# Kernel tuning notes

Hardware: AMD Instinct MI355X
Metric: run time of the kernel (lower is better)

Reference implementation:

```python
import jax, jax.numpy as jnp
import numpy as np

COLUMN_COUNT = 2048
CELLS_PER_COLUMN = 32
NUM_CELLS = COLUMN_COUNT * CELLS_PER_COLUMN
MAX_SEGMENTS = 16
MAX_SYNAPSES = 32
ACTIVATION_THRESHOLD = 13
PERMANENCE_CONNECTED = 0.5


def setup_inputs() -> dict:
    key = jax.random.key(0)
    k1, k2, k3, k4, k5 = jax.random.split(key, 5)
    active_columns = jax.random.randint(k1, (COLUMN_COUNT,), 0, 2).astype(jnp.float32)
    prev_active = jax.random.randint(k2, (NUM_CELLS,), 0, 2).astype(jnp.float32)
    prev_predictive = jax.random.randint(k3, (NUM_CELLS,), 0, 2).astype(jnp.float32)
    seg_pre = jax.random.randint(k4, (NUM_CELLS, MAX_SEGMENTS, MAX_SYNAPSES), 0, NUM_CELLS, dtype=jnp.int32)
    seg_perm = jax.random.uniform(k5, (NUM_CELLS, MAX_SEGMENTS, MAX_SYNAPSES), dtype=jnp.float32)
    return {
        'active_columns': active_columns,
        'prev_active': prev_active,
        'prev_predictive': prev_predictive,
        'seg_pre': seg_pre,
        'seg_perm': seg_perm,
    }


def _best_segment_activity(seg_pre, connected, active_vec):
    """Per cell: max over segments of (# synapses that are connected AND whose
    presynaptic cell is active). Mirrors _get_segment_activity/_get_best_matching_segment."""
    pre_active = active_vec[seg_pre] > 0          # [N, S, K] irregular gather
    counts = jnp.sum(connected & pre_active, axis=-1)  # [N, S]
    return jnp.max(counts, axis=-1)               # [N]


def reference(active_columns, prev_active, prev_predictive, seg_pre, seg_perm):
    C, cpc = COLUMN_COUNT, CELLS_PER_COLUMN
    connected = seg_perm >= PERMANENCE_CONNECTED   # [N, S, K]

    col_active = active_columns > 0                           # [C]
    pred = (prev_predictive > 0).reshape(C, cpc)              # [C, cpc]
    col_has_pred = jnp.any(pred, axis=1)                      # [C]

    # Active cells: predicted cells if any prediction in column, else burst (all cells).
    new_active = jnp.where(col_active[:, None],
                           jnp.where(col_has_pred[:, None], pred, True),
                           False)                             # [C, cpc]
    active_flat = new_active.reshape(-1).astype(jnp.float32)  # [N]

    # New predictive cells: any segment with activity >= activation_threshold
    # w.r.t. the NEW active set.
    best_act = _best_segment_activity(seg_pre, connected, active_flat)  # [N]
    new_predictive = (best_act >= ACTIVATION_THRESHOLD).astype(jnp.float32)

    # Anomaly: fraction of active columns with no predicted cell.
    n_active_cols = jnp.sum(col_active)
    n_predicted = jnp.sum(col_active & col_has_pred)
    anomaly = (1.0 - n_predicted / jnp.maximum(n_active_cols, 1)).astype(jnp.float32)

    return active_flat, new_predictive, anomaly


if __name__ == '__main__':
    out = reference(**setup_inputs())
    print([o.shape for o in out])
```

## Files before the change

kernel.cpp:

```cpp
#include <hip/hip_runtime.h>

#define COLS    2048
#define CPC     32
#define NCELLS  65536
#define SEGS    16
#define SYN     32
#define THRESH  13

#define CPW     16
#define CPB     (4 * CPW)
#define PREDICT_GRID (NCELLS / CPB)

__global__ __launch_bounds__(256) void tm_active_kernel(
    const float* __restrict__ active_columns,
    const float* __restrict__ prev_predictive,
    float* __restrict__ out_active,
    unsigned int* __restrict__ ws_mask,
    unsigned char* __restrict__ ws_flags)
{
    int n = blockIdx.x * 256 + threadIdx.x;
    int c = n >> 5;
    int j = n & 31;
    int lane = threadIdx.x & 63;

    bool predbit    = prev_predictive[n] > 0.0f;
    bool col_active = active_columns[c] > 0.0f;

    unsigned long long pb = __ballot(predbit);
    unsigned int colmask = (lane < 32) ? (unsigned int)pb : (unsigned int)(pb >> 32);
    bool has_pred = (colmask != 0u);

    bool active = col_active && (has_pred ? predbit : true);
    out_active[n] = active ? 1.0f : 0.0f;

    unsigned long long ab = __ballot(active);
    if (lane == 0)  ws_mask[c] = (unsigned int)ab;
    if (lane == 32) ws_mask[c] = (unsigned int)(ab >> 32);

    if (j == 0)
        ws_flags[c] = (unsigned char)((col_active ? 1 : 0) |
                                      ((col_active && has_pred) ? 2 : 0));
}

typedef const __attribute__((address_space(1))) void* gas_ptr;
typedef __attribute__((address_space(3)))       void* las_ptr;

__device__ __forceinline__ void dma_1kb(const char* g, char* lds, int lane) {
    __builtin_amdgcn_global_load_lds((gas_ptr)(g + lane * 16), (las_ptr)lds, 16, 0, 0);
}

__global__ __launch_bounds__(256) void tm_predict_kernel(
    const int*   __restrict__ seg_pre,
    const float* __restrict__ seg_perm,
    const unsigned int* __restrict__ ws_mask,
    const unsigned char* __restrict__ ws_flags,
    float* __restrict__ out_pred,
    float* __restrict__ out_anomaly)
{
    __shared__ unsigned int mask[COLS];
    __shared__ char stage[4][2][4096];

    int tid  = threadIdx.x;
    int wave = tid >> 6;
    int lane = tid & 63;
    int base = blockIdx.x * CPB + wave * CPW;

    {
        const char* gp = (const char*)(seg_pre  + (size_t)base * 512);
        const char* gq = (const char*)(seg_perm + (size_t)base * 512);
        char* L = stage[wave][0];
        dma_1kb(gp,        L,        lane);
        dma_1kb(gp + 1024, L + 1024, lane);
        dma_1kb(gq,        L + 2048, lane);
        dma_1kb(gq + 1024, L + 3072, lane);
    }

    ((uint4*)mask)[tid]       = ((const uint4*)ws_mask)[tid];
    ((uint4*)mask)[tid + 256] = ((const uint4*)ws_mask)[tid + 256];

    __syncthreads();

    unsigned pmask = 0;
    #pragma unroll
    for (int i = 0; i < CPW; ++i) {
        char* L = stage[wave][i & 1];

        if (i + 1 < CPW) {
            asm volatile("s_waitcnt lgkmcnt(0)" ::: "memory");
            const char* gp = (const char*)(seg_pre  + (size_t)(base + i + 1) * 512);
            const char* gq = (const char*)(seg_perm + (size_t)(base + i + 1) * 512);
            char* Ln = stage[wave][(i + 1) & 1];
            dma_1kb(gp,        Ln,        lane);
            dma_1kb(gp + 1024, Ln + 1024, lane);
            dma_1kb(gq,        Ln + 2048, lane);
            dma_1kb(gq + 1024, Ln + 3072, lane);
            __builtin_amdgcn_sched_barrier(0);
            asm volatile("s_waitcnt vmcnt(4)" ::: "memory");
        } else {
            asm volatile("s_waitcnt vmcnt(0)" ::: "memory");
        }

        const int4*   pl = (const int4*)  L;
        const float4* ql = (const float4*)(L + 2048);

        int4   p0 = pl[lane], p1 = pl[lane + 64];
        float4 q0 = ql[lane], q1 = ql[lane + 64];

        int c0 = 0, c1 = 0;
        c0 += (q0.x >= 0.5f && ((mask[(unsigned)p0.x >> 5] >> ((unsigned)p0.x & 31u)) & 1u)) ? 1 : 0;
        c0 += (q0.y >= 0.5f && ((mask[(unsigned)p0.y >> 5] >> ((unsigned)p0.y & 31u)) & 1u)) ? 1 : 0;
        c0 += (q0.z >= 0.5f && ((mask[(unsigned)p0.z >> 5] >> ((unsigned)p0.z & 31u)) & 1u)) ? 1 : 0;
        c0 += (q0.w >= 0.5f && ((mask[(unsigned)p0.w >> 5] >> ((unsigned)p0.w & 31u)) & 1u)) ? 1 : 0;
        c1 += (q1.x >= 0.5f && ((mask[(unsigned)p1.x >> 5] >> ((unsigned)p1.x & 31u)) & 1u)) ? 1 : 0;
        c1 += (q1.y >= 0.5f && ((mask[(unsigned)p1.y >> 5] >> ((unsigned)p1.y & 31u)) & 1u)) ? 1 : 0;
        c1 += (q1.z >= 0.5f && ((mask[(unsigned)p1.z >> 5] >> ((unsigned)p1.z & 31u)) & 1u)) ? 1 : 0;
        c1 += (q1.w >= 0.5f && ((mask[(unsigned)p1.w >> 5] >> ((unsigned)p1.w & 31u)) & 1u)) ? 1 : 0;

        int v = c0 | (c1 << 16);
        v += __shfl_xor(v, 1, 64);
        v += __shfl_xor(v, 2, 64);
        v += __shfl_xor(v, 4, 64);
        int m = max(v & 0xffff, v >> 16);
        m = max(m, __shfl_xor(m, 8, 64));
        m = max(m, __shfl_xor(m, 16, 64));
        m = max(m, __shfl_xor(m, 32, 64));

        pmask |= (m >= THRESH) ? (1u << i) : 0u;
    }

    if (lane < CPW)
        out_pred[base + lane] = ((pmask >> lane) & 1u) ? 1.0f : 0.0f;

    if (blockIdx.x == 0 && tid < 64) {
        const unsigned int* f = (const unsigned int*)ws_flags;
        int na = 0, np = 0;
        #pragma unroll
        for (int i = 0; i < 8; ++i) {
            unsigned w = f[tid * 8 + i];
            na += __popc(w & 0x01010101u);
            np += __popc(w & 0x02020202u);
        }
        int v = na | (np << 16);
        v += __shfl_xor(v, 1, 64);
        v += __shfl_xor(v, 2, 64);
        v += __shfl_xor(v, 4, 64);
        v += __shfl_xor(v, 8, 64);
        v += __shfl_xor(v, 16, 64);
        v += __shfl_xor(v, 32, 64);
        if (tid == 0) {
            int NA = v & 0xffff, NP = v >> 16;
            *out_anomaly = 1.0f - (float)NP / (float)(NA > 1 ? NA : 1);
        }
    }
}

extern "C" void kernel_launch(void* const* d_in, const int* in_sizes, int n_in,
                              void* d_out, int out_size, void* d_ws, size_t ws_size,
                              hipStream_t stream) {
    const float* active_columns  = (const float*)d_in[0];
    const float* prev_predictive = (const float*)d_in[2];
    const int*   seg_pre         = (const int*)d_in[3];
    const float* seg_perm        = (const float*)d_in[4];
    float* out = (float*)d_out;

    unsigned int*  ws_mask  = (unsigned int*)d_ws;
    unsigned char* ws_flags = (unsigned char*)d_ws + COLS * sizeof(unsigned int);

    tm_active_kernel<<<NCELLS / 256, 256, 0, stream>>>(
        active_columns, prev_predictive, out, ws_mask, ws_flags);

    tm_predict_kernel<<<PREDICT_GRID, 256, 0, stream>>>(
        seg_pre, seg_perm, ws_mask, ws_flags,
        out + NCELLS, out + 2 * NCELLS);
}
```

Baseline: 287.1 us.

## Replace LDS DMA staging with register double-buffered nontemporal loads

Drops the global_load_lds staging buffers and the per-cell waitcnt pipeline in the predict kernel. Each wave now loads segment indices and permanences straight into registers, two cells at a time, with A/B register double buffering so the next pair's loads overlap the current pair's counting. Permanence loads use nontemporal hints, and launch bounds request 4 blocks per CU. This removes the LDS round-trip and the explicit waits, but raises register pressure, which could limit occupancy or cause spills.

```diff
diff --git a/kernel.cpp b/kernel.cpp
--- a/kernel.cpp
+++ b/kernel.cpp
@@ -42,14 +42,42 @@
                                       ((col_active && has_pred) ? 2 : 0));
 }
 
-typedef const __attribute__((address_space(1))) void* gas_ptr;
-typedef __attribute__((address_space(3)))       void* las_ptr;
+typedef int   i4 __attribute__((ext_vector_type(4)));
+typedef float f4 __attribute__((ext_vector_type(4)));
 
-__device__ __forceinline__ void dma_1kb(const char* g, char* lds, int lane) {
-    __builtin_amdgcn_global_load_lds((gas_ptr)(g + lane * 16), (las_ptr)lds, 16, 0, 0);
+__device__ __forceinline__ int cell_count(const unsigned int* mask,
+                                          i4 p0, i4 p1, f4 q0, f4 q1)
+{
+    int c0 = 0, c1 = 0;
+    c0 += (q0.x >= 0.5f && ((mask[(unsigned)p0.x >> 5] >> ((unsigned)p0.x & 31u)) & 1u)) ? 1 : 0;
+    c0 += (q0.y >= 0.5f && ((mask[(unsigned)p0.y >> 5] >> ((unsigned)p0.y & 31u)) & 1u)) ? 1 : 0;
+    c0 += (q0.z >= 0.5f && ((mask[(unsigned)p0.z >> 5] >> ((unsigned)p0.z & 31u)) & 1u)) ? 1 : 0;
+    c0 += (q0.w >= 0.5f && ((mask[(unsigned)p0.w >> 5] >> ((unsigned)p0.w & 31u)) & 1u)) ? 1 : 0;
+    c1 += (q1.x >= 0.5f && ((mask[(unsigned)p1.x >> 5] >> ((unsigned)p1.x & 31u)) & 1u)) ? 1 : 0;
+    c1 += (q1.y >= 0.5f && ((mask[(unsigned)p1.y >> 5] >> ((unsigned)p1.y & 31u)) & 1u)) ? 1 : 0;
+    c1 += (q1.z >= 0.5f && ((mask[(unsigned)p1.z >> 5] >> ((unsigned)p1.z & 31u)) & 1u)) ? 1 : 0;
+    c1 += (q1.w >= 0.5f && ((mask[(unsigned)p1.w >> 5] >> ((unsigned)p1.w & 31u)) & 1u)) ? 1 : 0;
+
+    int v = c0 | (c1 << 16);
+    v += __shfl_xor(v, 1, 64);
+    v += __shfl_xor(v, 2, 64);
+    v += __shfl_xor(v, 4, 64);
+    int m = max(v & 0xffff, v >> 16);
+    m = max(m, __shfl_xor(m, 8, 64));
+    m = max(m, __shfl_xor(m, 16, 64));
+    m = max(m, __shfl_xor(m, 32, 64));
+    return m;
 }
 
-__global__ __launch_bounds__(256) void tm_predict_kernel(
+#define LOADPAIR(P0,P1,P2,P3,Q0,Q1,Q2,Q3, cell) do {                         \
+    const i4* _p = gp + (cell) * 128;                                        \
+    const f4* _q = gq + (cell) * 128;                                        \
+    P0 = _p[0];   P1 = _p[64];   P2 = _p[128];  P3 = _p[192];                \
+    Q0 = __builtin_nontemporal_load(_q);        Q1 = __builtin_nontemporal_load(_q + 64); \
+    Q2 = __builtin_nontemporal_load(_q + 128);  Q3 = __builtin_nontemporal_load(_q + 192); \
+} while (0)
+
+__global__ __launch_bounds__(256, 4) void tm_predict_kernel(
     const int*   __restrict__ seg_pre,
     const float* __restrict__ seg_perm,
     const unsigned int* __restrict__ ws_mask,
@@ -58,22 +86,19 @@
     float* __restrict__ out_anomaly)
 {
     __shared__ unsigned int mask[COLS];
-    __shared__ char stage[4][2][4096];
 
     int tid  = threadIdx.x;
     int wave = tid >> 6;
     int lane = tid & 63;
     int base = blockIdx.x * CPB + wave * CPW;
 
-    {
-        const char* gp = (const char*)(seg_pre  + (size_t)base * 512);
-        const char* gq = (const char*)(seg_perm + (size_t)base * 512);
-        char* L = stage[wave][0];
-        dma_1kb(gp,        L,        lane);
-        dma_1kb(gp + 1024, L + 1024, lane);
-        dma_1kb(gq,        L + 2048, lane);
-        dma_1kb(gq + 1024, L + 3072, lane);
-    }
+    const i4* gp = (const i4*)(seg_pre  + (size_t)base * 512) + lane;
+    const f4* gq = (const f4*)(seg_perm + (size_t)base * 512) + lane;
+
+    i4 pA0, pA1, pA2, pA3, pB0, pB1, pB2, pB3;
+    f4 qA0, qA1, qA2, qA3, qB0, qB1, qB2, qB3;
+
+    LOADPAIR(pA0,pA1,pA2,pA3,qA0,qA1,qA2,qA3, 0);
 
     ((uint4*)mask)[tid]       = ((const uint4*)ws_mask)[tid];
     ((uint4*)mask)[tid + 256] = ((const uint4*)ws_mask)[tid + 256];
@@ -82,50 +107,21 @@
 
     unsigned pmask = 0;
     #pragma unroll
-    for (int i = 0; i < CPW; ++i) {
-        char* L = stage[wave][i & 1];
+    for (int j = 0; j < 8; j += 2) {
+        LOADPAIR(pB0,pB1,pB2,pB3,qB0,qB1,qB2,qB3, 2*(j+1));
 
-        if (i + 1 < CPW) {
-            asm volatile("s_waitcnt lgkmcnt(0)" ::: "memory");
-            const char* gp = (const char*)(seg_pre  + (size_t)(base + i + 1) * 512);
-            const char* gq = (const char*)(seg_perm + (size_t)(base + i + 1) * 512);
-            char* Ln = stage[wave][(i + 1) & 1];
-            dma_1kb(gp,        Ln,        lane);
-            dma_1kb(gp + 1024, Ln + 1024, lane);
-            dma_1kb(gq,        Ln + 2048, lane);
-            dma_1kb(gq + 1024, Ln + 3072, lane);
-            __builtin_amdgcn_sched_barrier(0);
-            asm volatile("s_waitcnt vmcnt(4)" ::: "memory");
-        } else {
-            asm volatile("s_waitcnt vmcnt(0)" ::: "memory");
-        }
+        int m0 = cell_count(mask, pA0, pA1, qA0, qA1);
+        int m1 = cell_count(mask, pA2, pA3, qA2, qA3);
+        pmask |= (m0 >= THRESH) ? (1u << (2*j))     : 0u;
+        pmask |= (m1 >= THRESH) ? (1u << (2*j + 1)) : 0u;
 
-        const int4*   pl = (const int4*)  L;
-        const float4* ql = (const float4*)(L + 2048);
+        if (j + 2 < 8)
+            LOADPAIR(pA0,pA1,pA2,pA3,qA0,qA1,qA2,qA3, 2*(j+2));
 
-        int4   p0 = pl[lane], p1 = pl[lane + 64];
-        float4 q0 = ql[lane], q1 = ql[lane + 64];
-
-        int c0 = 0, c1 = 0;
-        c0 += (q0.x >= 0.5f && ((mask[(unsigned)p0.x >> 5] >> ((unsigned)p0.x & 31u)) & 1u)) ? 1 : 0;
-        c0 += (q0.y >= 0.5f && ((mask[(unsigned)p0.y >> 5] >> ((unsigned)p0.y & 31u)) & 1u)) ? 1 : 0;
-        c0 += (q0.z >= 0.5f && ((mask[(unsigned)p0.z >> 5] >> ((unsigned)p0.z & 31u)) & 1u)) ? 1 : 0;
-        c0 += (q0.w >= 0.5f && ((mask[(unsigned)p0.w >> 5] >> ((unsigned)p0.w & 31u)) & 1u)) ? 1 : 0;
-        c1 += (q1.x >= 0.5f && ((mask[(unsigned)p1.x >> 5] >> ((unsigned)p1.x & 31u)) & 1u)) ? 1 : 0;
-        c1 += (q1.y >= 0.5f && ((mask[(unsigned)p1.y >> 5] >> ((unsigned)p1.y & 31u)) & 1u)) ? 1 : 0;
-        c1 += (q1.z >= 0.5f && ((mask[(unsigned)p1.z >> 5] >> ((unsigned)p1.z & 31u)) & 1u)) ? 1 : 0;
-        c1 += (q1.w >= 0.5f && ((mask[(unsigned)p1.w >> 5] >> ((unsigned)p1.w & 31u)) & 1u)) ? 1 : 0;
-
-        int v = c0 | (c1 << 16);
-        v += __shfl_xor(v, 1, 64);
-        v += __shfl_xor(v, 2, 64);
-        v += __shfl_xor(v, 4, 64);
-        int m = max(v & 0xffff, v >> 16);
-        m = max(m, __shfl_xor(m, 8, 64));
-        m = max(m, __shfl_xor(m, 16, 64));
-        m = max(m, __shfl_xor(m, 32, 64));
-
-        pmask |= (m >= THRESH) ? (1u << i) : 0u;
+        int m2 = cell_count(mask, pB0, pB1, qB0, qB1);
+        int m3 = cell_count(mask, pB2, pB3, qB2, qB3);
+        pmask |= (m2 >= THRESH) ? (1u << (2*j + 2)) : 0u;
+        pmask |= (m3 >= THRESH) ? (1u << (2*j + 3)) : 0u;
     }
 
     if (lane < CPW)
```

Result: faster. 273.6 us (-4.7%).
